# Kernel optimization log

Hardware: AMD Instinct MI355X
Metric: run time of the kernel (lower is better)

The kernel has to match this reference:

```python
import jax, jax.numpy as jnp
import numpy as np


def setup_inputs() -> dict:
    key = jax.random.key(0)
    k1, k2, k3 = jax.random.split(key, 3)
    B, Cin, Cout, L, K = 16, 64, 64, 65536, 3
    return {
        "x": jax.random.normal(k1, (B, Cin, L), dtype=jnp.float32),
        "alpha": jnp.zeros((1, Cin, 1), dtype=jnp.float32),
        "weight": jax.random.normal(k2, (Cout, Cin, K), dtype=jnp.float32),
        "weight_scale": jnp.ones((Cout, 1, 1), dtype=jnp.float32),
        "bias": jax.random.normal(k3, (Cout,), dtype=jnp.float32),
        "beta": jnp.ones((1, Cout, 1), dtype=jnp.float32),
        "gamma": jnp.zeros((1, Cout, 1), dtype=jnp.float32),
        "zeta": jnp.zeros((1, Cout, 1), dtype=jnp.float32),
    }


def _rsign(x, alpha):
    # forward: sign(x - alpha) in {-1,+1}; backward: identity w.r.t. x (STE)
    signed = jnp.where(x >= alpha, 1.0, -1.0).astype(x.dtype)
    return x + jax.lax.stop_gradient(signed - x)


def _clipped_ste_sign(w):
    # forward: sign(w); backward: grad passes only where |w| <= 1 (Bi-RealNet)
    w_bin = jnp.sign(w)
    mask = (jnp.abs(w) <= 1.0).astype(w.dtype)
    wm = w * mask
    return jax.lax.stop_gradient(w_bin) + wm - jax.lax.stop_gradient(wm)


def _rprelu(x, beta, gamma, zeta):
    xs = x - gamma
    return jnp.where(x > gamma, xs + zeta, beta * xs + zeta)


def reference(x, alpha, weight, weight_scale, bias, beta, gamma, zeta):
    # RSign -> scaled binary conv1d (stride=1, pad=1) -> RPReLU
    xb = _rsign(x, alpha)                        # [B,Cin,L], values +-1
    wb = _clipped_ste_sign(weight) * weight_scale  # [Cout,Cin,K]
    y = jax.lax.conv_general_dilated(
        xb, wb, window_strides=(1,), padding=[(1, 1)],
        dimension_numbers=("NCH", "OIH", "NCH"))  # [B,Cout,L]
    y = y + bias[None, :, None]
    return _rprelu(y, beta, gamma, zeta)
```

## Files before the change

### kernel.cpp

```cpp
#include <hip/hip_runtime.h>

#define LLEN 65536
#define CIN 64
#define COUT 64
#define LTILE 1024

typedef float f32x4 __attribute__((ext_vector_type(4)));
typedef unsigned long long u64;

#define BROW (LLEN + 2)

struct __align__(64) WRec {
    u64 p0, p1, p2;
    float A;
    float S;
    float Bv, G, Z;
    float f0, f2;
    float pad[3];
};

__global__ void pack_weights(const float* __restrict__ w,
                             const float* __restrict__ wscale,
                             const float* __restrict__ bias,
                             const float* __restrict__ beta,
                             const float* __restrict__ gamma,
                             const float* __restrict__ zeta,
                             WRec* __restrict__ rec) {
    int co = threadIdx.x;
    if (co >= COUT) return;
    u64 p[3];
    int nnz[3], ntot = 0;
    for (int k = 0; k < 3; ++k) {
        u64 pos = 0ull, nz = 0ull;
        for (int ci = 0; ci < CIN; ++ci) {
            float wv = w[co * (CIN * 3) + ci * 3 + k];
            pos |= ((u64)(wv > 0.0f)) << ci;
            nz  |= ((u64)(wv != 0.0f)) << ci;
        }
        p[k] = pos;
        nnz[k] = __popcll(nz);
        ntot += nnz[k];
    }
    WRec r;
    float s = wscale[co];
    r.p0 = p[0]; r.p1 = p[1]; r.p2 = p[2];
    r.A  = s * (float)ntot + bias[co];
    r.S  = -2.0f * s;
    r.Bv = beta[co]; r.G = gamma[co]; r.Z = zeta[co];
    r.f0 = 0.5f * (float)nnz[0];
    r.f2 = 0.5f * (float)nnz[2];
    r.pad[0] = r.pad[1] = r.pad[2] = 0.0f;
    rec[co] = r;
}

__global__ void __launch_bounds__(256) pack_x(
        const float* __restrict__ x,
        const float* __restrict__ alpha,
        u64* __restrict__ bits) {
    const int t = threadIdx.x;
    const int b = blockIdx.y;
    const int l0 = blockIdx.x * LTILE + 4 * t;
    const float* xb = x + (size_t)b * CIN * LLEN + l0;

    u64 w0 = 0, w1 = 0, w2 = 0, w3 = 0;
    #pragma unroll 16
    for (int ci = 0; ci < CIN; ++ci) {
        const f32x4 v = *(const f32x4*)(xb + (size_t)ci * LLEN);
        const float a = alpha[ci];
        w0 |= ((u64)(v.x >= a)) << ci;
        w1 |= ((u64)(v.y >= a)) << ci;
        w2 |= ((u64)(v.z >= a)) << ci;
        w3 |= ((u64)(v.w >= a)) << ci;
    }
    u64* dst = bits + (size_t)b * BROW + l0 + 1;
    dst[0] = w0; dst[1] = w1; dst[2] = w2; dst[3] = w3;
}

__device__ __forceinline__ float rprelu(float y, float B, float G, float Z) {
    float xs = y - G;
    return (y > G) ? (xs + Z) : fmaf(B, xs, Z);
}

template <int EDGE>
__device__ __forceinline__ void co_loop(const WRec* __restrict__ rec,
                                        u64 xq0, u64 xq1, u64 xq2,
                                        u64 xq3, u64 xq4, u64 xq5,
                                        bool fixlane, float* __restrict__ outp) {
    #pragma unroll 4
    for (int co = 0; co < COUT; ++co) {
        const WRec r = rec[co];
        float fx = (float)(__popcll(xq0 ^ r.p0) + __popcll(xq1 ^ r.p1)
                         + __popcll(xq2 ^ r.p2));
        float fy = (float)(__popcll(xq1 ^ r.p0) + __popcll(xq2 ^ r.p1)
                         + __popcll(xq3 ^ r.p2));
        float fz = (float)(__popcll(xq2 ^ r.p0) + __popcll(xq3 ^ r.p1)
                         + __popcll(xq4 ^ r.p2));
        float fw = (float)(__popcll(xq3 ^ r.p0) + __popcll(xq4 ^ r.p1)
                         + __popcll(xq5 ^ r.p2));
        if (EDGE == 1 && fixlane)
            fx = (float)(__popcll(xq1 ^ r.p1) + __popcll(xq2 ^ r.p2)) + r.f0;
        if (EDGE == 2 && fixlane)
            fw = (float)(__popcll(xq3 ^ r.p0) + __popcll(xq4 ^ r.p1)) + r.f2;
        f32x4 o;
        o.x = rprelu(fmaf(r.S, fx, r.A), r.Bv, r.G, r.Z);
        o.y = rprelu(fmaf(r.S, fy, r.A), r.Bv, r.G, r.Z);
        o.z = rprelu(fmaf(r.S, fz, r.A), r.Bv, r.G, r.Z);
        o.w = rprelu(fmaf(r.S, fw, r.A), r.Bv, r.G, r.Z);
        __builtin_nontemporal_store(o, (f32x4*)(outp + (size_t)co * LLEN));
    }
}

__global__ void __launch_bounds__(256) bconv_compute(
        const u64* __restrict__ bits,
        const WRec* __restrict__ rec,
        float* __restrict__ out) {
    const int t = threadIdx.x;
    const int b = blockIdx.y;
    const int l0 = blockIdx.x * LTILE + 4 * t;

    const u64* src = bits + (size_t)b * BROW + l0;
    const u64 xq0 = src[0], xq1 = src[1], xq2 = src[2],
              xq3 = src[3], xq4 = src[4], xq5 = src[5];

    float* outp = out + (size_t)b * COUT * LLEN + l0;

    if (blockIdx.x == 0)
        co_loop<1>(rec, xq0, xq1, xq2, xq3, xq4, xq5, t == 0, outp);
    else if (blockIdx.x == gridDim.x - 1)
        co_loop<2>(rec, xq0, xq1, xq2, xq3, xq4, xq5, t == 255, outp);
    else
        co_loop<0>(rec, xq0, xq1, xq2, xq3, xq4, xq5, false, outp);
}

extern "C" void kernel_launch(void* const* d_in, const int* in_sizes, int n_in,
                              void* d_out, int out_size, void* d_ws, size_t ws_size,
                              hipStream_t stream) {
    const float* x      = (const float*)d_in[0];
    const float* alpha  = (const float*)d_in[1];
    const float* w      = (const float*)d_in[2];
    const float* wscale = (const float*)d_in[3];
    const float* bias   = (const float*)d_in[4];
    const float* beta   = (const float*)d_in[5];
    const float* gamma  = (const float*)d_in[6];
    const float* zeta   = (const float*)d_in[7];
    float* out = (float*)d_out;

    WRec* rec = (WRec*)d_ws;
    u64* bits = (u64*)((char*)d_ws + 4096);

    pack_weights<<<1, 64, 0, stream>>>(w, wscale, bias, beta, gamma, zeta, rec);

    dim3 grid(LLEN / LTILE, 16);
    pack_x<<<grid, 256, 0, stream>>>(x, alpha, bits);
    bconv_compute<<<grid, 256, 0, stream>>>(bits, rec, out);
}
```

Baseline: 121.6 us.

## Remap conv grid to per-output-channel blocks and narrow pack_x loads

```diff
diff --git a/kernel.cpp b/kernel.cpp
--- a/kernel.cpp
+++ b/kernel.cpp
@@ -3,8 +3,8 @@
 #define LLEN 65536
 #define CIN 64
 #define COUT 64
-#define LTILE 1024
 
+typedef float f32x2 __attribute__((ext_vector_type(2)));
 typedef float f32x4 __attribute__((ext_vector_type(4)));
 typedef unsigned long long u64;
 
@@ -59,21 +59,26 @@
         u64* __restrict__ bits) {
     const int t = threadIdx.x;
     const int b = blockIdx.y;
-    const int l0 = blockIdx.x * LTILE + 4 * t;
+    const int l0 = blockIdx.x * 512 + 2 * t;
     const float* xb = x + (size_t)b * CIN * LLEN + l0;
 
-    u64 w0 = 0, w1 = 0, w2 = 0, w3 = 0;
-    #pragma unroll 16
-    for (int ci = 0; ci < CIN; ++ci) {
-        const f32x4 v = *(const f32x4*)(xb + (size_t)ci * LLEN);
-        const float a = alpha[ci];
-        w0 |= ((u64)(v.x >= a)) << ci;
-        w1 |= ((u64)(v.y >= a)) << ci;
-        w2 |= ((u64)(v.z >= a)) << ci;
-        w3 |= ((u64)(v.w >= a)) << ci;
+    u64 w0 = 0, w1 = 0;
+    #pragma unroll
+    for (int q = 0; q < 4; ++q) {
+        f32x2 buf[16];
+        #pragma unroll
+        for (int j = 0; j < 16; ++j)
+            buf[j] = *(const f32x2*)(xb + (size_t)(q * 16 + j) * LLEN);
+        #pragma unroll
+        for (int j = 0; j < 16; ++j) {
+            const int ci = q * 16 + j;
+            const float a = alpha[ci];
+            w0 |= ((u64)(buf[j].x >= a)) << ci;
+            w1 |= ((u64)(buf[j].y >= a)) << ci;
+        }
     }
     u64* dst = bits + (size_t)b * BROW + l0 + 1;
-    dst[0] = w0; dst[1] = w1; dst[2] = w2; dst[3] = w3;
+    dst[0] = w0; dst[1] = w1;
 }
 
 __device__ __forceinline__ float rprelu(float y, float B, float G, float Z) {
@@ -81,14 +86,30 @@
     return (y > G) ? (xs + Z) : fmaf(B, xs, Z);
 }
 
-template <int EDGE>
-__device__ __forceinline__ void co_loop(const WRec* __restrict__ rec,
-                                        u64 xq0, u64 xq1, u64 xq2,
-                                        u64 xq3, u64 xq4, u64 xq5,
-                                        bool fixlane, float* __restrict__ outp) {
+__global__ void __launch_bounds__(256) bconv_compute(
+        const u64* __restrict__ bits,
+        const WRec* __restrict__ rec,
+        float* __restrict__ out) {
+    const int t     = threadIdx.x;
+    const int co    = blockIdx.x;
+    const int chunk = blockIdx.y;
+    const int b     = blockIdx.z;
+    const int c0    = chunk * 8192;
+
+    const WRec r = rec[co];
+    const u64* bb = bits + (size_t)b * BROW + c0;
+    float* outp = out + ((size_t)b * COUT + co) * LLEN + c0 + 4 * t;
+
+    const bool lo = (chunk == 0) && (t == 0);
+    const bool hi = (chunk == 7) && (t == 255);
+
     #pragma unroll 4
-    for (int co = 0; co < COUT; ++co) {
-        const WRec r = rec[co];
+    for (int j = 0; j < 8; ++j) {
+        const int l0 = 1024 * j + 4 * t;
+        const u64* src = bb + l0;
+        const u64 xq0 = src[0], xq1 = src[1], xq2 = src[2],
+                  xq3 = src[3], xq4 = src[4], xq5 = src[5];
+
         float fx = (float)(__popcll(xq0 ^ r.p0) + __popcll(xq1 ^ r.p1)
                          + __popcll(xq2 ^ r.p2));
         float fy = (float)(__popcll(xq1 ^ r.p0) + __popcll(xq2 ^ r.p1)
@@ -97,39 +118,18 @@
                          + __popcll(xq4 ^ r.p2));
         float fw = (float)(__popcll(xq3 ^ r.p0) + __popcll(xq4 ^ r.p1)
                          + __popcll(xq5 ^ r.p2));
-        if (EDGE == 1 && fixlane)
+        if (j == 0 && lo)
             fx = (float)(__popcll(xq1 ^ r.p1) + __popcll(xq2 ^ r.p2)) + r.f0;
-        if (EDGE == 2 && fixlane)
+        if (j == 7 && hi)
             fw = (float)(__popcll(xq3 ^ r.p0) + __popcll(xq4 ^ r.p1)) + r.f2;
+
         f32x4 o;
         o.x = rprelu(fmaf(r.S, fx, r.A), r.Bv, r.G, r.Z);
         o.y = rprelu(fmaf(r.S, fy, r.A), r.Bv, r.G, r.Z);
         o.z = rprelu(fmaf(r.S, fz, r.A), r.Bv, r.G, r.Z);
         o.w = rprelu(fmaf(r.S, fw, r.A), r.Bv, r.G, r.Z);
-        __builtin_nontemporal_store(o, (f32x4*)(outp + (size_t)co * LLEN));
+        __builtin_nontemporal_store(o, (f32x4*)(outp + 1024 * j));
     }
-}
-
-__global__ void __launch_bounds__(256) bconv_compute(
-        const u64* __restrict__ bits,
-        const WRec* __restrict__ rec,
-        float* __restrict__ out) {
-    const int t = threadIdx.x;
-    const int b = blockIdx.y;
-    const int l0 = blockIdx.x * LTILE + 4 * t;
-
-    const u64* src = bits + (size_t)b * BROW + l0;
-    const u64 xq0 = src[0], xq1 = src[1], xq2 = src[2],
-              xq3 = src[3], xq4 = src[4], xq5 = src[5];
-
-    float* outp = out + (size_t)b * COUT * LLEN + l0;
-
-    if (blockIdx.x == 0)
-        co_loop<1>(rec, xq0, xq1, xq2, xq3, xq4, xq5, t == 0, outp);
-    else if (blockIdx.x == gridDim.x - 1)
-        co_loop<2>(rec, xq0, xq1, xq2, xq3, xq4, xq5, t == 255, outp);
-    else
-        co_loop<0>(rec, xq0, xq1, xq2, xq3, xq4, xq5, false, outp);
 }
 
 extern "C" void kernel_launch(void* const* d_in, const int* in_sizes, int n_in,
@@ -150,7 +150,9 @@
 
     pack_weights<<<1, 64, 0, stream>>>(w, wscale, bias, beta, gamma, zeta, rec);
 
-    dim3 grid(LLEN / LTILE, 16);
-    pack_x<<<grid, 256, 0, stream>>>(x, alpha, bits);
-    bconv_compute<<<grid, 256, 0, stream>>>(bits, rec, out);
+    dim3 gridA(LLEN / 512, 16);
+    pack_x<<<gridA, 256, 0, stream>>>(x, alpha, bits);
+
+    dim3 gridB(COUT, 8, 16);
+    bconv_compute<<<gridB, 256, 0, stream>>>(bits, rec, out);
 }
```

Result: faster. 104.9 us (-13.7%).
